# Kernel tuning notes

Hardware: AMD Instinct MI355X
Metric: run time of the kernel (lower is better)

Reference implementation:

```python
import jax, jax.numpy as jnp
import numpy as np

SLICES = [(12, 1), (13, 1)]  # (input_width, hidden_size=1) per slice


def _lstm_last_hidden(xs, W_ih, W_hh, b):
    """Run a standard (PyTorch gate order i,f,g,o) LSTM over time, return last h.
    xs: [T, B, in]; W_ih: [4*H, in]; W_hh: [4*H, H]; b: [4*H] (b_ih + b_hh).
    Returns h_T: [B, H].
    """
    B = xs.shape[1]
    H = W_hh.shape[1]
    h0 = jnp.zeros((B, H), xs.dtype)
    c0 = jnp.zeros((B, H), xs.dtype)

    def step(carry, xt):
        h, c = carry
        gates = xt @ W_ih.T + h @ W_hh.T + b  # [B, 4H]
        i, f, g, o = jnp.split(gates, 4, axis=-1)
        i = jax.nn.sigmoid(i)
        f = jax.nn.sigmoid(f)
        g = jnp.tanh(g)
        o = jax.nn.sigmoid(o)
        c = f * c + i * g
        h = o * jnp.tanh(c)
        return (h, c), None

    (hT, _), _ = jax.lax.scan(step, (h0, c0), xs)
    return hT


def setup_inputs() -> dict:
    key = jax.random.key(0)
    ks = jax.random.split(key, 9)
    B, T, F = 4096, 512, 25
    nb_out = 1
    s = 0.1
    x = jax.random.normal(ks[0], (B, T, F), dtype=jnp.float32)
    # slice-1 LSTM (input 12, hidden 1)
    W_ih1 = jax.random.normal(ks[1], (4, 12), dtype=jnp.float32) * s
    W_hh1 = jax.random.normal(ks[2], (4, 1), dtype=jnp.float32) * s
    b1 = jax.random.normal(ks[3], (4,), dtype=jnp.float32) * s
    # slice-2 LSTM (input 13, hidden 1)
    W_ih2 = jax.random.normal(ks[4], (4, 13), dtype=jnp.float32) * s
    W_hh2 = jax.random.normal(ks[5], (4, 1), dtype=jnp.float32) * s
    b2 = jax.random.normal(ks[6], (4,), dtype=jnp.float32) * s
    # output head Linear(2, nb_out)
    W_out = jax.random.normal(ks[7], (nb_out, 2), dtype=jnp.float32) * s
    b_out = jax.random.normal(ks[8], (nb_out,), dtype=jnp.float32) * s
    return {"x": x, "W_ih1": W_ih1, "W_hh1": W_hh1, "b1": b1,
            "W_ih2": W_ih2, "W_hh2": W_hh2, "b2": b2,
            "W_out": W_out, "b_out": b_out}


def reference(x, W_ih1, W_hh1, b1, W_ih2, W_hh2, b2, W_out, b_out):
    # x: [B, T, 25] -> time-major [T, B, 25]
    xs = jnp.transpose(x, (1, 0, 2))
    h1 = _lstm_last_hidden(xs[..., :12], W_ih1, W_hh1, b1)   # [B, 1]
    h2 = _lstm_last_hidden(xs[..., 12:], W_ih2, W_hh2, b2)   # [B, 1]
    h = jnp.concatenate([h1, h2], axis=-1)                   # [B, 2] == lstm_out[:, -1, :]
    out = h @ W_out.T + b_out                                # [B, nb_out]
    return jax.nn.sigmoid(out)
```

## Files before the change

kernel.cpp:

```cpp
#include <hip/hip_runtime.h>
#include <stdint.h>


#define T_STEPS 512
#define F_IN    25
#define TC      16
#define NTILES  (T_STEPS / TC)
#define CH      2
#define XROW    520
#define ZROW    136
#define XBUF    (CH * XROW)
#define ZBUF    (CH * ZROW)
#define LOG2E   1.44269504088896340736f

typedef const __attribute__((address_space(1))) void* as1_cvp;
typedef __attribute__((address_space(3)))       void* as3_vp;

__device__ __forceinline__ void gll16(const float* gsrc, const float* ldst) {
  __builtin_amdgcn_global_load_lds((as1_cvp)(uintptr_t)gsrc,
                                   (as3_vp)(uint32_t)(uintptr_t)ldst, 16, 0, 0);
}

__device__ __forceinline__ float sigm(float v) {
  return __builtin_amdgcn_rcpf(1.0f + __builtin_amdgcn_exp2f(v * (-LOG2E)));
}
__device__ __forceinline__ float tanh_(float v) {
  return fmaf(2.0f, __builtin_amdgcn_rcpf(1.0f + __builtin_amdgcn_exp2f(v * (-2.0f * LOG2E))), -1.0f);
}

__device__ __forceinline__ void prefetch_tile(const float* __restrict__ x, int b0, int tile,
                                              float* xbuf, int lane) {
  const float* base = x + (size_t)b0 * (T_STEPS * F_IN) + tile * (TC * F_IN);
  const int i1 = lane * 4;
  int i2 = 256 + lane * 4;
  if (i2 > 396) i2 = 396;
#pragma unroll
  for (int cc = 0; cc < CH; ++cc) {
    const float* g0 = base + cc * (T_STEPS * F_IN);
    gll16(g0 + i1, xbuf + cc * XROW);
    gll16(g0 + i2, xbuf + cc * XROW + 256);
  }
}

__device__ __forceinline__ void gemv_tile(const float* __restrict__ xbuf, float* __restrict__ zbuf,
                                          int c, int lt, int xoff, int zoff,
                                          const float* __restrict__ w, const float* __restrict__ zb) {
  const float* xr = xbuf + c * XROW + lt * F_IN + xoff;
  float z0 = zb[0], z1 = zb[1], z2 = zb[2], z3 = zb[3];
#pragma unroll
  for (int f = 0; f < 13; ++f) {
    const float xv = xr[f];
    z0 = fmaf(w[0 * 13 + f], xv, z0);
    z1 = fmaf(w[1 * 13 + f], xv, z1);
    z2 = fmaf(w[2 * 13 + f], xv, z2);
    z3 = fmaf(w[3 * 13 + f], xv, z3);
  }
  *(float4*)(zbuf + c * ZROW + lt * 8 + zoff) = make_float4(z0, z1, z2, z3);
}

__device__ __forceinline__ void scan_tile(const float* __restrict__ zbuf, int c, int zoff,
                                          const float* __restrict__ whh, float& hv, float& cv) {
#pragma unroll
  for (int t = 0; t < TC; ++t) {
    const float4 z4 = *(const float4*)(zbuf + c * ZROW + t * 8 + zoff);
    const float pi = fmaf(hv, whh[0], z4.x);
    const float pf = fmaf(hv, whh[1], z4.y);
    const float pg = fmaf(hv, whh[2], z4.z);
    const float po = fmaf(hv, whh[3], z4.w);
    const float ai = sigm(pi);
    const float af = sigm(pf);
    const float ag = tanh_(pg);
    const float ao = sigm(po);
    cv = fmaf(af, cv, ai * ag);
    hv = ao * tanh_(cv);
  }
}

__global__ void __launch_bounds__(64, 2)
lstm2_fused(const float* __restrict__ x,
            const float* __restrict__ Wih1, const float* __restrict__ Whh1, const float* __restrict__ b1,
            const float* __restrict__ Wih2, const float* __restrict__ Whh2, const float* __restrict__ b2,
            const float* __restrict__ Wout, const float* __restrict__ bout,
            float* __restrict__ out)
{
  __shared__ __align__(16) float xs[3 * XBUF];
  __shared__ __align__(16) float zs[2 * ZBUF];

  const int lane = threadIdx.x;
  const int c    = lane >> 5;
  const int lt   = lane & 15;
  const int half = (lane >> 4) & 1;
  const int xoff = half * 12;
  const int zoff = half * 4;
  const int b0   = blockIdx.x * CH;

  float w[52], zb[4], whh[4];
#pragma unroll
  for (int j = 0; j < 4; ++j) {
#pragma unroll
    for (int f = 0; f < 13; ++f) {
      const float wa = (f < 12) ? Wih1[j * 12 + f] : 0.0f;
      const float wb = Wih2[j * 13 + f];
      w[j * 13 + f] = half ? wb : wa;
    }
    zb[j]  = half ? b2[j]   : b1[j];
    whh[j] = half ? Whh2[j] : Whh1[j];
  }

  float hv = 0.0f, cv = 0.0f;

  prefetch_tile(x, b0, 0, xs + 0 * XBUF, lane);
  prefetch_tile(x, b0, 1, xs + 1 * XBUF, lane);
  prefetch_tile(x, b0, 2, xs + 2 * XBUF, lane);
  asm volatile("s_waitcnt vmcnt(8)" ::: "memory");
  gemv_tile(xs, zs, c, lt, xoff, zoff, w, zb);
  asm volatile("s_waitcnt lgkmcnt(0)" ::: "memory");

  int pb = 0;
  int rb = 1;
  for (int k = 0; k < NTILES - 1; ++k) {
    asm volatile("s_waitcnt vmcnt(4)" ::: "memory");
    int tn = k + 3;
    if (tn > NTILES - 1) tn = NTILES - 1;
    prefetch_tile(x, b0, tn, xs + pb * XBUF, lane);
    pb = (pb == 2) ? 0 : pb + 1;
    const float* zrd = zs + (k & 1) * ZBUF;
    float*       zwr = zs + ((k + 1) & 1) * ZBUF;
    const float* xrd = xs + rb * XBUF;
    rb = (rb == 2) ? 0 : rb + 1;
    scan_tile(zrd, c, zoff, whh, hv, cv);
    gemv_tile(xrd, zwr, c, lt, xoff, zoff, w, zb);
    asm volatile("s_waitcnt lgkmcnt(0)" ::: "memory");
  }
  scan_tile(zs + ZBUF, c, zoff, whh, hv, cv);
  asm volatile("s_waitcnt vmcnt(0)" ::: "memory");

  const float h1 = __shfl(hv, (lane & 32) + 0, 64);
  const float h2 = __shfl(hv, (lane & 32) + 16, 64);
  if ((lane & 31) == 0) {
    out[b0 + c] = sigm(fmaf(Wout[0], h1, fmaf(Wout[1], h2, bout[0])));
  }
}

extern "C" void kernel_launch(void* const* d_in, const int* in_sizes, int n_in,
                              void* d_out, int out_size, void* d_ws, size_t ws_size,
                              hipStream_t stream) {
  const float* x    = (const float*)d_in[0];
  const float* Wih1 = (const float*)d_in[1];
  const float* Whh1 = (const float*)d_in[2];
  const float* b1   = (const float*)d_in[3];
  const float* Wih2 = (const float*)d_in[4];
  const float* Whh2 = (const float*)d_in[5];
  const float* b2   = (const float*)d_in[6];
  const float* Wout = (const float*)d_in[7];
  const float* bout = (const float*)d_in[8];
  float* out = (float*)d_out;

  const int B = in_sizes[0] / (T_STEPS * F_IN);
  dim3 grid(B / CH), block(64);
  hipLaunchKernelGGL(lstm2_fused, grid, block, 0, stream,
                     x, Wih1, Whh1, b1, Wih2, Whh2, b2, Wout, bout, out);
}
```

Baseline: 309.9 us.

## Process four batch rows per wave with remapped gemv and scan lane roles

Each 64-lane block now handles four batch rows instead of two. The gemv is remapped so each lane computes two timesteps. The scan uses only 8 distinct lanes (4 rows x 2 LSTMs), replicated across the wave. This halves the grid and doubles the per-block prefetch volume, with vmcnt thresholds adjusted to match. It aims to amortize the serial recurrence latency over more rows per wave, but grid size drops and launch bounds now allow only one block per SIMD, so fewer waves are available to hide latency.

```diff
diff --git a/kernel.cpp b/kernel.cpp
--- a/kernel.cpp
+++ b/kernel.cpp
@@ -6,7 +6,7 @@
 #define F_IN    25
 #define TC      16
 #define NTILES  (T_STEPS / TC)
-#define CH      2
+#define CH      4
 #define XROW    520
 #define ZROW    136
 #define XBUF    (CH * XROW)
@@ -43,26 +43,30 @@
 }
 
 __device__ __forceinline__ void gemv_tile(const float* __restrict__ xbuf, float* __restrict__ zbuf,
-                                          int c, int lt, int xoff, int zoff,
+                                          int cg, int lt, int xoff, int zoff,
                                           const float* __restrict__ w, const float* __restrict__ zb) {
-  const float* xr = xbuf + c * XROW + lt * F_IN + xoff;
-  float z0 = zb[0], z1 = zb[1], z2 = zb[2], z3 = zb[3];
 #pragma unroll
-  for (int f = 0; f < 13; ++f) {
-    const float xv = xr[f];
-    z0 = fmaf(w[0 * 13 + f], xv, z0);
-    z1 = fmaf(w[1 * 13 + f], xv, z1);
-    z2 = fmaf(w[2 * 13 + f], xv, z2);
-    z3 = fmaf(w[3 * 13 + f], xv, z3);
+  for (int p = 0; p < 2; ++p) {
+    const int tl = p * 8 + lt;
+    const float* xr = xbuf + cg * XROW + tl * F_IN + xoff;
+    float z0 = zb[0], z1 = zb[1], z2 = zb[2], z3 = zb[3];
+#pragma unroll
+    for (int f = 0; f < 13; ++f) {
+      const float xv = xr[f];
+      z0 = fmaf(w[0 * 13 + f], xv, z0);
+      z1 = fmaf(w[1 * 13 + f], xv, z1);
+      z2 = fmaf(w[2 * 13 + f], xv, z2);
+      z3 = fmaf(w[3 * 13 + f], xv, z3);
+    }
+    *(float4*)(zbuf + cg * ZROW + tl * 8 + zoff) = make_float4(z0, z1, z2, z3);
   }
-  *(float4*)(zbuf + c * ZROW + lt * 8 + zoff) = make_float4(z0, z1, z2, z3);
 }
 
-__device__ __forceinline__ void scan_tile(const float* __restrict__ zbuf, int c, int zoff,
+__device__ __forceinline__ void scan_tile(const float* __restrict__ zbuf, int cs, int zoff,
                                           const float* __restrict__ whh, float& hv, float& cv) {
 #pragma unroll
   for (int t = 0; t < TC; ++t) {
-    const float4 z4 = *(const float4*)(zbuf + c * ZROW + t * 8 + zoff);
+    const float4 z4 = *(const float4*)(zbuf + cs * ZROW + t * 8 + zoff);
     const float pi = fmaf(hv, whh[0], z4.x);
     const float pf = fmaf(hv, whh[1], z4.y);
     const float pg = fmaf(hv, whh[2], z4.z);
@@ -76,7 +80,7 @@
   }
 }
 
-__global__ void __launch_bounds__(64, 2)
+__global__ void __launch_bounds__(64, 1)
 lstm2_fused(const float* __restrict__ x,
             const float* __restrict__ Wih1, const float* __restrict__ Whh1, const float* __restrict__ b1,
             const float* __restrict__ Wih2, const float* __restrict__ Whh2, const float* __restrict__ b2,
@@ -87,11 +91,14 @@
   __shared__ __align__(16) float zs[2 * ZBUF];
 
   const int lane = threadIdx.x;
-  const int c    = lane >> 5;
-  const int lt   = lane & 15;
-  const int half = (lane >> 4) & 1;
-  const int xoff = half * 12;
-  const int zoff = half * 4;
+  const int cg   = lane >> 4;
+  const int hg   = (lane >> 3) & 1;
+  const int lt   = lane & 7;
+  const int xoff = hg * 12;
+  const int zofg = hg * 4;
+  const int cs   = lane & 3;
+  const int hs   = (lane >> 2) & 1;
+  const int zofs = hs * 4;
   const int b0   = blockIdx.x * CH;
 
   float w[52], zb[4], whh[4];
@@ -101,10 +108,10 @@
     for (int f = 0; f < 13; ++f) {
       const float wa = (f < 12) ? Wih1[j * 12 + f] : 0.0f;
       const float wb = Wih2[j * 13 + f];
-      w[j * 13 + f] = half ? wb : wa;
+      w[j * 13 + f] = hg ? wb : wa;
     }
-    zb[j]  = half ? b2[j]   : b1[j];
-    whh[j] = half ? Whh2[j] : Whh1[j];
+    zb[j]  = hg ? b2[j]   : b1[j];
+    whh[j] = hs ? Whh2[j] : Whh1[j];
   }
 
   float hv = 0.0f, cv = 0.0f;
@@ -112,14 +119,14 @@
   prefetch_tile(x, b0, 0, xs + 0 * XBUF, lane);
   prefetch_tile(x, b0, 1, xs + 1 * XBUF, lane);
   prefetch_tile(x, b0, 2, xs + 2 * XBUF, lane);
-  asm volatile("s_waitcnt vmcnt(8)" ::: "memory");
-  gemv_tile(xs, zs, c, lt, xoff, zoff, w, zb);
+  asm volatile("s_waitcnt vmcnt(16)" ::: "memory");
+  gemv_tile(xs, zs, cg, lt, xoff, zofg, w, zb);
   asm volatile("s_waitcnt lgkmcnt(0)" ::: "memory");
 
   int pb = 0;
   int rb = 1;
   for (int k = 0; k < NTILES - 1; ++k) {
-    asm volatile("s_waitcnt vmcnt(4)" ::: "memory");
+    asm volatile("s_waitcnt vmcnt(8)" ::: "memory");
     int tn = k + 3;
     if (tn > NTILES - 1) tn = NTILES - 1;
     prefetch_tile(x, b0, tn, xs + pb * XBUF, lane);
@@ -128,17 +135,17 @@
     float*       zwr = zs + ((k + 1) & 1) * ZBUF;
     const float* xrd = xs + rb * XBUF;
     rb = (rb == 2) ? 0 : rb + 1;
-    scan_tile(zrd, c, zoff, whh, hv, cv);
-    gemv_tile(xrd, zwr, c, lt, xoff, zoff, w, zb);
+    scan_tile(zrd, cs, zofs, whh, hv, cv);
+    gemv_tile(xrd, zwr, cg, lt, xoff, zofg, w, zb);
     asm volatile("s_waitcnt lgkmcnt(0)" ::: "memory");
   }
-  scan_tile(zs + ZBUF, c, zoff, whh, hv, cv);
+  scan_tile(zs + ZBUF, cs, zofs, whh, hv, cv);
   asm volatile("s_waitcnt vmcnt(0)" ::: "memory");
 
-  const float h1 = __shfl(hv, (lane & 32) + 0, 64);
-  const float h2 = __shfl(hv, (lane & 32) + 16, 64);
-  if ((lane & 31) == 0) {
-    out[b0 + c] = sigm(fmaf(Wout[0], h1, fmaf(Wout[1], h2, bout[0])));
+  const float h1 = __shfl(hv, (lane & 3), 64);
+  const float h2 = __shfl(hv, (lane & 3) + 4, 64);
+  if (lane < 4) {
+    out[b0 + lane] = sigm(fmaf(Wout[0], h1, fmaf(Wout[1], h2, bout[0])));
   }
 }
 
```

Result: no change. 307.1 us (-0.9%).
